# Optimization experiments

Measured on AMD Instinct MI355X. Metric: run time of the kernel, lower is better.

## Reference

```python
import jax, jax.numpy as jnp
import numpy as np

B, T, C, H, S = 4, 1024, 768, 12, 64  # batch, seq, emb_dim, n_heads, head_size
FF = 4 * C          # 3072, ff_hidden_size (required by SwiGLU input dim)
HID = int(8 * C / 3)  # 2048, SwiGLU hidden
EPS = 1e-6


def _rope_tables(seq_len, dim):
    # theta = 10000 ** (-2 * arange(0, dim, 2) / dim)  (note extra factor 2 vs standard RoPE)
    theta = 10000.0 ** (-2.0 * jnp.arange(0, dim, 2, dtype=jnp.float32) / dim)
    freqs = jnp.arange(seq_len, dtype=jnp.float32)[:, None] * theta  # [T, dim/2]
    cos = jnp.repeat(jnp.cos(freqs), 2, axis=-1)  # [T, dim]
    sin = jnp.repeat(jnp.sin(freqs), 2, axis=-1)
    return cos, sin


def _rope(x, cos, sin):
    # x: [..., T, S]; rotate pairs: even' = -odd, odd' = even
    rot = jnp.stack([-x[..., 1::2], x[..., 0::2]], axis=-1).reshape(x.shape)
    return x * cos + rot * sin


def _rmsnorm(x, gamma):
    # global scalar RMS over the whole tensor (faithful to torch.mean with no dim)
    return x / jnp.sqrt(EPS + jnp.mean(x * x)) * gamma


def _block(x, Wq, Wk, Wv, Wo, g1, g2, W1, b1, Ww, bw, Wg, bg, Wd, bd, W2, b2):
    Tlen = x.shape[1]
    cos, sin = _rope_tables(Tlen, S)
    # --- multi-head attention on rms1(x) ---
    h = _rmsnorm(x, g1)
    q = jnp.einsum('btc,hcs->bhts', h, Wq)
    k = jnp.einsum('btc,hcs->bhts', h, Wk)
    v = jnp.einsum('btc,hcs->bhts', h, Wv)
    rq = _rope(q, cos, sin)
    rk = _rope(k, cos, sin)
    scores = jnp.einsum('bhts,bhks->bhtk', rq, rk) * (C ** -0.5)  # scale by emb_dim, faithful
    causal = jnp.tril(jnp.ones((Tlen, Tlen), dtype=bool))
    scores = jnp.where(causal, scores, -jnp.inf)
    probs = jax.nn.softmax(scores, axis=-1)
    attn = jnp.einsum('bhtk,bhks->bhts', probs, v)
    attn = attn.transpose(0, 2, 1, 3).reshape(x.shape[0], Tlen, C)  # concat heads
    out = x + attn @ Wo
    # --- feed forward on rms2(out) ---
    h2 = _rmsnorm(out, g2)
    u = h2 @ W1 + b1                      # [B,T,FF]
    wx = u @ Ww + bw                      # [B,T,HID]
    vx = u @ Wg + bg
    ff = (wx * (vx * jax.nn.sigmoid(vx))) @ Wd + bd  # [B,T,FF]
    ff = ff @ W2 + b2                     # [B,T,C]
    return out + ff


def setup_inputs() -> dict:
    key = jax.random.key(0)
    ks = jax.random.split(key, 17)
    sd = 0.02
    return {
        'x':  jax.random.normal(ks[0], (B, T, C), jnp.float32),
        'Wq': jax.random.normal(ks[1], (H, C, S), jnp.float32) * sd,
        'Wk': jax.random.normal(ks[2], (H, C, S), jnp.float32) * sd,
        'Wv': jax.random.normal(ks[3], (H, C, S), jnp.float32) * sd,
        'Wo': jax.random.normal(ks[4], (C, C), jnp.float32) * sd,
        'g1': jnp.ones((C,), jnp.float32),
        'g2': jnp.ones((C,), jnp.float32),
        'W1': jax.random.normal(ks[5], (C, FF), jnp.float32) * sd,
        'b1': jnp.zeros((FF,), jnp.float32),
        'Ww': jax.random.normal(ks[6], (FF, HID), jnp.float32) * sd,
        'bw': jnp.zeros((HID,), jnp.float32),
        'Wg': jax.random.normal(ks[7], (FF, HID), jnp.float32) * sd,
        'bg': jnp.zeros((HID,), jnp.float32),
        'Wd': jax.random.normal(ks[8], (HID, FF), jnp.float32) * sd,
        'bd': jnp.zeros((FF,), jnp.float32),
        'W2': jax.random.normal(ks[9], (FF, C), jnp.float32) * sd,
        'b2': jnp.zeros((C,), jnp.float32),
    }


def reference(x, Wq, Wk, Wv, Wo, g1, g2, W1, b1, Ww, bw, Wg, bg, Wd, bd, W2, b2):
    return _block(x, Wq, Wk, Wv, Wo, g1, g2, W1, b1, Ww, bw, Wg, bg, Wd, bd, W2, b2)
```

## Files before the change

### kernel.cpp

```cpp
#include <hip/hip_runtime.h>
#include <math.h>

#define BB   4
#define TT   1024
#define CC   768
#define HH   12
#define SS   64
#define FFD  3072
#define HIDD 2048
#define NTOK (BB*TT)
#define EPSR 1e-6f

typedef __attribute__((ext_vector_type(8))) short bf16x8;
typedef __attribute__((ext_vector_type(4))) float f32x4;

__device__ __forceinline__ unsigned short f2bf(float f) {
    unsigned u = __float_as_uint(f);
    return (unsigned short)((u + 0x7FFFu + ((u >> 16) & 1u)) >> 16);
}
__device__ __forceinline__ float bfl(unsigned u) { return __uint_as_float(u << 16); }
__device__ __forceinline__ float bfh(unsigned u) { return __uint_as_float(u & 0xFFFF0000u); }
__device__ __forceinline__ unsigned pk2(float a, float b) {
    return (unsigned)f2bf(a) | ((unsigned)f2bf(b) << 16);
}

__device__ __forceinline__ void gload_lds16(const unsigned short* g, unsigned short* l) {
    __builtin_amdgcn_global_load_lds(
        (const __attribute__((address_space(1))) unsigned int*)g,
        (__attribute__((address_space(3))) unsigned int*)l, 16, 0, 0);
}

__global__ void k_sumsq_partial(const float* __restrict__ x, float* __restrict__ part, int n4) {
    __shared__ float sm[256];
    float s = 0.f;
    int stride = gridDim.x * blockDim.x;
    for (int i = blockIdx.x * blockDim.x + threadIdx.x; i < n4; i += stride) {
        float4 v = ((const float4*)x)[i];
        s += v.x*v.x + v.y*v.y + v.z*v.z + v.w*v.w;
    }
    sm[threadIdx.x] = s;
    __syncthreads();
    for (int off = 128; off > 0; off >>= 1) {
        if (threadIdx.x < off) sm[threadIdx.x] += sm[threadIdx.x + off];
        __syncthreads();
    }
    if (threadIdx.x == 0) part[blockIdx.x] = sm[0];
}

__global__ void k_scale_gamma_b(const float* __restrict__ x, const float* __restrict__ g,
                                const float* __restrict__ part, unsigned short* __restrict__ h,
                                int n8, float invn) {
    __shared__ float sm[256];
    float s = 0.f;
#pragma unroll
    for (int k = 0; k < 4; ++k) s += part[threadIdx.x + k*256];
    sm[threadIdx.x] = s;
    __syncthreads();
    for (int off = 128; off > 0; off >>= 1) {
        if (threadIdx.x < off) sm[threadIdx.x] += sm[threadIdx.x + off];
        __syncthreads();
    }
    float sc = 1.0f / sqrtf(EPSR + sm[0] * invn);
    int i = blockIdx.x * blockDim.x + threadIdx.x;
    if (i >= n8) return;
    float4 v0 = ((const float4*)x)[2*i];
    float4 v1 = ((const float4*)x)[2*i+1];
    int c = (i * 8) % CC;
    float4 g0 = *(const float4*)(g + c);
    float4 g1v = *(const float4*)(g + c + 4);
    uint4 r;
    r.x = pk2(v0.x*sc*g0.x,  v0.y*sc*g0.y);
    r.y = pk2(v0.z*sc*g0.z,  v0.w*sc*g0.w);
    r.z = pk2(v1.x*sc*g1v.x, v1.y*sc*g1v.y);
    r.w = pk2(v1.z*sc*g1v.z, v1.w*sc*g1v.w);
    ((uint4*)h)[i] = r;
}

#define TQKV 1728
#define TWO  576
#define TW1  2304
#define TWW  6144
#define TWD  6144
#define TW2  2304
#define J0 (TQKV)
#define J1 (J0 + TWO)
#define J2 (J1 + TW1)
#define J3 (J2 + TWW)
#define J4 (J3 + TWW)
#define J5 (J4 + TWD)
#define J6 (J5 + TW2)
#define J7 (J6 + 16)
#define J8 (J7 + 128)

__device__ __forceinline__ void wT_tile(float (*tl)[33], const float* __restrict__ W,
                                        unsigned short* __restrict__ Wt,
                                        int K, int N, int t, int tx, int ty) {
    int nk = K >> 5;
    int k0 = (t % nk) * 32, n0 = (t / nk) * 32;
#pragma unroll
    for (int i = 0; i < 4; ++i)
        tl[ty + i*8][tx] = W[(size_t)(k0 + ty + i*8) * N + n0 + tx];
    __syncthreads();
#pragma unroll
    for (int i = 0; i < 4; ++i)
        Wt[(size_t)(n0 + ty + i*8) * K + k0 + tx] = f2bf(tl[tx][ty + i*8]);
}

__global__ void k_prep(const float* __restrict__ Wq, const float* __restrict__ Wk,
                       const float* __restrict__ Wv, const float* __restrict__ Wo,
                       const float* __restrict__ W1, const float* __restrict__ Ww,
                       const float* __restrict__ Wg, const float* __restrict__ Wd,
                       const float* __restrict__ W2, const float* __restrict__ bw,
                       const float* __restrict__ bg,
                       unsigned short* __restrict__ wqkvT, unsigned short* __restrict__ WoT,
                       unsigned short* __restrict__ W1T, unsigned short* __restrict__ WcatT,
                       unsigned short* __restrict__ WdT, unsigned short* __restrict__ W2T,
                       float* __restrict__ bcat, float* __restrict__ tab) {
    __shared__ float tl[32][33];
    const int bid = blockIdx.x;
    const int tx = threadIdx.x & 31, ty = threadIdx.x >> 5;
    if (bid < J0) {
        int t = bid;
        int c0 = (t % 24) * 32;
        int s0 = ((t / 24) & 1) * 32;
        int z = t / 48, sel = z / HH, h = z % HH;
        const float* W = (sel == 0 ? Wq : (sel == 1 ? Wk : Wv)) + (size_t)h * CC * SS;
#pragma unroll
        for (int i = 0; i < 4; ++i)
            tl[ty + i*8][tx] = W[(size_t)(c0 + ty + i*8) * SS + s0 + tx];
        __syncthreads();
#pragma unroll
        for (int i = 0; i < 4; ++i)
            wqkvT[(size_t)(sel*CC + h*SS + s0 + ty + i*8) * CC + c0 + tx] = f2bf(tl[tx][ty + i*8]);
    } else if (bid < J1) {
        wT_tile(tl, Wo, WoT, CC, CC, bid - J0, tx, ty);
    } else if (bid < J2) {
        wT_tile(tl, W1, W1T, CC, FFD, bid - J1, tx, ty);
    } else if (bid < J3) {
        wT_tile(tl, Ww, WcatT, FFD, HIDD, bid - J2, tx, ty);
    } else if (bid < J4) {
        wT_tile(tl, Wg, WcatT + (size_t)HIDD*FFD, FFD, HIDD, bid - J3, tx, ty);
    } else if (bid < J5) {
        wT_tile(tl, Wd, WdT, HIDD, FFD, bid - J4, tx, ty);
    } else if (bid < J6) {
        wT_tile(tl, W2, W2T, FFD, CC, bid - J5, tx, ty);
    } else if (bid < J7) {
        int i = (bid - J6) * 256 + threadIdx.x;
        bcat[i] = (i < HIDD) ? bw[i] : bg[i - HIDD];
    } else {
        int i = (bid - J7) * 256 + threadIdx.x;
        int t = i >> 5, j = i & 31;
        float th = expf(-(float)j * 0.5756462732485115f);
        float ang = (float)t * th;
        tab[2*i]   = cosf(ang);
        tab[2*i+1] = sinf(ang);
    }
}

__global__ void k_rope_vt(unsigned short* __restrict__ qkv, const float* __restrict__ tab,
                          unsigned short* __restrict__ vtg) {
    const int bid = blockIdx.x;
    if (bid < 6144) {
        int i = bid * 256 + threadIdx.x;
        int j  = i & 31;
        int h  = (i >> 5) % HH;
        int bt = i / (32 * HH);
        int t  = bt & (TT - 1);
        float cs = tab[(t*32 + j)*2];
        float sn = tab[(t*32 + j)*2 + 1];
        size_t base = (size_t)bt * (3*CC) + h * SS + 2*j;
        unsigned q = *(unsigned*)(qkv + base);
        float qe = bfl(q), qo = bfh(q);
        *(unsigned*)(qkv + base) = pk2(qe*cs - qo*sn, qo*cs + qe*sn);
        unsigned k = *(unsigned*)(qkv + base + CC);
        float ke = bfl(k), ko = bfh(k);
        *(unsigned*)(qkv + base + CC) = pk2(ke*cs - ko*sn, ko*cs + ke*sn);
    } else {
        int b2 = bid - 6144;
        int bh = b2 >> 3, ty = b2 & 7;
        int b = bh / HH, h = bh % HH;
        int d = threadIdx.x & 63, tq = threadIdx.x >> 6;
        int t0 = ty * 128 + tq * 32;
        const unsigned short* src = qkv + (size_t)(b*TT + t0)*(3*CC) + 2*CC + h*SS + d;
        unsigned v[16];
#pragma unroll
        for (int e = 0; e < 16; ++e) {
            unsigned lo = src[(size_t)(2*e)*(3*CC)];
            unsigned hi = src[(size_t)(2*e+1)*(3*CC)];
            v[e] = (lo & 0xFFFFu) | (hi << 16);
        }
        uint4* dst = (uint4*)(vtg + ((size_t)bh*64 + d)*TT + t0);
#pragma unroll
        for (int q = 0; q < 4; ++q)
            dst[q] = make_uint4(v[q*4], v[q*4+1], v[q*4+2], v[q*4+3]);
    }
}

template<bool BIAS, bool RES, bool OUTB>
__global__ __launch_bounds__(256) void k_gemm_bf16(
    const unsigned short* __restrict__ A, const unsigned short* __restrict__ Bt,
    const float* __restrict__ bias, const float* __restrict__ res,
    void* __restrict__ Cv, int M, int N, int K)
{
    __shared__ unsigned short As[2][128*32];
    __shared__ unsigned short Bs[2][128*32];
    const int tid  = threadIdx.x;
    const int w    = tid >> 6, lane = tid & 63;
    const int wr   = w >> 1,  wc   = w & 1;
    const int row0 = blockIdx.y * 128, col0 = blockIdx.x * 128;

    f32x4 acc[4][4];
#pragma unroll
    for (int m = 0; m < 4; ++m)
#pragma unroll
        for (int n = 0; n < 4; ++n) acc[m][n] = (f32x4){0.f, 0.f, 0.f, 0.f};

    const int lr4 = lane >> 2;
    const int scb = lane & 3;

    auto stage = [&](int t, int buf) {
#pragma unroll
        for (int i = 0; i < 2; ++i) {
            int lr = w * 32 + i * 16 + lr4;
            int cbs = scb ^ ((lr >> 1) & 3);
            const unsigned short* ga = A + (size_t)(row0 + lr) * K + t * 32 + cbs * 8;
            gload_lds16(ga, &As[buf][(w * 32 + i * 16) * 32]);
            const unsigned short* gb = Bt + (size_t)(col0 + lr) * K + t * 32 + cbs * 8;
            gload_lds16(gb, &Bs[buf][(w * 32 + i * 16) * 32]);
        }
    };

    const int nt = K / 32;
    stage(0, 0);
    int cur = 0;
    const int fr = lane & 15, fq = lane >> 4;
    for (int t = 0; t < nt; ++t) {
        __syncthreads();
        if (t + 1 < nt) stage(t + 1, cur ^ 1);
        bf16x8 af[4], bf[4];
#pragma unroll
        for (int m = 0; m < 4; ++m) {
            int ra = wr * 64 + m * 16 + fr;
            af[m] = *(const bf16x8*)&As[cur][ra * 32 + (fq ^ ((ra >> 1) & 3)) * 8];
            int rb = wc * 64 + m * 16 + fr;
            bf[m] = *(const bf16x8*)&Bs[cur][rb * 32 + (fq ^ ((rb >> 1) & 3)) * 8];
        }
#pragma unroll
        for (int m = 0; m < 4; ++m)
#pragma unroll
            for (int n = 0; n < 4; ++n)
                acc[m][n] = __builtin_amdgcn_mfma_f32_16x16x32_bf16(af[m], bf[n], acc[m][n], 0, 0, 0);
        cur ^= 1;
    }

#pragma unroll
    for (int m = 0; m < 4; ++m) {
#pragma unroll
        for (int n = 0; n < 4; ++n) {
            int col = col0 + wc * 64 + n * 16 + fr;
            float bv = BIAS ? bias[col] : 0.f;
#pragma unroll
            for (int j = 0; j < 4; ++j) {
                int row = row0 + wr * 64 + m * 16 + fq * 4 + j;
                size_t off = (size_t)row * N + col;
                float v = acc[m][n][j] + bv;
                if (RES) v += res[off];
                if (OUTB) ((unsigned short*)Cv)[off] = f2bf(v);
                else      ((float*)Cv)[off] = v;
            }
        }
    }
}

#define GSTEP(s_, DOSTAGE, GATE)                                                  \
    {                                                                             \
        const int st_ = (s_) & 3;                                                 \
        const unsigned short* pa_ = &ringA[st_][0];                               \
        const unsigned short* pb_ = &ringB[st_][0];                               \
        bf16x8 af[8], bv[4];                                                      \
        _Pragma("unroll")                                                         \
        for (int m = 0; m < 8; ++m) {                                             \
            int ra = wm*128 + m*16 + fr;                                          \
            af[m] = *(const bf16x8*)&pa_[ra*32 + (fq ^ ((ra>>1)&3))*8];           \
        }                                                                         \
        _Pragma("unroll")                                                         \
        for (int n = 0; n < 4; ++n) {                                             \
            int rb = wn*64 + n*16 + fr;                                           \
            bv[n] = *(const bf16x8*)&pb_[rb*32 + (fq ^ ((rb>>1)&3))*8];           \
        }                                                                         \
        if (DOSTAGE) { stageA((s_) + 3); stageB((s_) + 3); }                      \
        asm volatile("s_waitcnt lgkmcnt(0)" ::: "memory");                        \
        __builtin_amdgcn_sched_barrier(0);                                        \
        __builtin_amdgcn_s_setprio(1);                                            \
        _Pragma("unroll")                                                         \
        for (int m = 0; m < 8; ++m)                                               \
            _Pragma("unroll")                                                     \
            for (int n = 0; n < 4; ++n)                                           \
                acc[m][n] = __builtin_amdgcn_mfma_f32_16x16x32_bf16(              \
                    af[m], bv[n], acc[m][n], 0, 0, 0);                            \
        __builtin_amdgcn_s_setprio(0);                                            \
        asm volatile("s_waitcnt " GATE ::: "memory");                             \
        __builtin_amdgcn_sched_barrier(0);                                        \
        __builtin_amdgcn_s_barrier();                                             \
    }

template<bool BIAS>
__global__ __launch_bounds__(512, 2) void k_gemm256(
    const unsigned short* __restrict__ A, const unsigned short* __restrict__ Bt,
    const float* __restrict__ bias, unsigned short* __restrict__ C,
    int M, int N, int K)
{
    __shared__ __align__(16) unsigned short ringA[4][256*32];
    __shared__ __align__(16) unsigned short ringB[4][256*32];
    const int tid = threadIdx.x;
    const int w = tid >> 6, lane = tid & 63;
    const int wm = w >> 2, wn = w & 3;
    const int fr = lane & 15, fq = lane >> 4;

    const int nwg = gridDim.x * gridDim.y;
    const int bid = blockIdx.y * gridDim.x + blockIdx.x;
    const int cpx = nwg >> 3;
    const int sbid = (bid & 7) * cpx + (bid >> 3);
    const int row0 = (sbid / gridDim.x) * 256;
    const int col0 = (sbid % gridDim.x) * 256;

    f32x4 acc[8][4];
#pragma unroll
    for (int m = 0; m < 8; ++m)
#pragma unroll
        for (int n = 0; n < 4; ++n) acc[m][n] = (f32x4){0.f, 0.f, 0.f, 0.f};

    auto stageA = [&](int t) {
        const int st = t & 3;
        const int kb = t * 32;
#pragma unroll
        for (int q = 0; q < 2; ++q) {
            int c = q * 512 + tid;
            int r = c >> 2;
            int part = (c & 3) ^ ((r >> 1) & 3);
            gload_lds16(A + (size_t)(row0 + r) * K + kb + part * 8,
                        &ringA[st][(q*512 + w*64) * 8]);
        }
    };
    auto stageB = [&](int t) {
        const int st = t & 3;
        const int kb = t * 32;
#pragma unroll
        for (int q = 0; q < 2; ++q) {
            int c = q * 512 + tid;
            int r = c >> 2;
            int part = (c & 3) ^ ((r >> 1) & 3);
            gload_lds16(Bt + (size_t)(col0 + r) * K + kb + part * 8,
                        &ringB[st][(q*512 + w*64) * 8]);
        }
    };

    const int S = K >> 5;
    stageA(0); stageB(0); stageA(1); stageB(1); stageA(2); stageB(2);
    asm volatile("s_waitcnt vmcnt(8)" ::: "memory");
    __builtin_amdgcn_s_barrier();
    int s = 0;
    for (; s < S - 3; ++s) GSTEP(s, true, "vmcnt(8)");
    GSTEP(s, false, "vmcnt(4)"); ++s;
    GSTEP(s, false, "vmcnt(0)"); ++s;
    GSTEP(s, false, "vmcnt(0)");

#pragma unroll
    for (int m = 0; m < 8; ++m) {
#pragma unroll
        for (int n = 0; n < 4; ++n) {
            int col = col0 + wn*64 + n*16 + fr;
            float bvb = BIAS ? bias[col] : 0.f;
#pragma unroll
            for (int j = 0; j < 4; ++j) {
                int row = row0 + wm*128 + m*16 + fq*4 + j;
                C[(size_t)row * N + col] = f2bf(acc[m][n][j] + bvb);
            }
        }
    }
}

__global__ __launch_bounds__(256) void k_attn_mfma(
    const unsigned short* __restrict__ qkv, const unsigned short* __restrict__ vtg,
    unsigned short* __restrict__ attn)
{
    __shared__ __align__(16) unsigned short Ks[2][64*64];
    __shared__ __align__(16) unsigned short Vs[2][64*64];
    __shared__ __align__(16) unsigned short Ps[4][16*72];
    const int tid = threadIdx.x;
    const int w = tid >> 6, lane = tid & 63;
    const int fr = lane & 15, fq = lane >> 4;
    const int bh = blockIdx.x, b = bh / HH, h = bh % HH;
    const int qb = blockIdx.y * 64;
    const int nkt = qb / 64 + 1;
    const float scale = 0.03608439182435161f;

    bf16x8 qf[2];
    {
        const unsigned short* qp = qkv + (size_t)(b*TT + qb + w*16 + fr)*(3*CC) + h*SS + fq*8;
        qf[0] = *(const bf16x8*)qp;
        qf[1] = *(const bf16x8*)(qp + 32);
    }

    auto stage = [&](int kt, int buf) {
        const unsigned short* kbase = qkv + (size_t)(b*TT + kt*64)*(3*CC) + CC + h*SS;
        const unsigned short* vbase = vtg + ((size_t)bh*64)*TT + kt*64;
#pragma unroll
        for (int p = 0; p < 2; ++p) {
            int s = p*256 + tid;
            int row = s >> 3;
            int blk = (s & 7) ^ (row & 7);
            gload_lds16(kbase + (size_t)row*(3*CC) + blk*8, &Ks[buf][(p*256 + w*64)*8]);
            gload_lds16(vbase + (size_t)row*TT + blk*8,     &Vs[buf][(p*256 + w*64)*8]);
        }
    };

    float m[4] = {-INFINITY, -INFINITY, -INFINITY, -INFINITY};
    float l[4] = {0.f, 0.f, 0.f, 0.f};
    f32x4 oacc[4];
#pragma unroll
    for (int n = 0; n < 4; ++n) oacc[n] = (f32x4){0.f, 0.f, 0.f, 0.f};

    stage(0, 0);
    int cur = 0;
    for (int kt = 0; kt < nkt; ++kt) {
        __syncthreads();
        if (kt + 1 < nkt) stage(kt + 1, cur ^ 1);

        f32x4 sacc[4];
#pragma unroll
        for (int n = 0; n < 4; ++n) sacc[n] = (f32x4){0.f, 0.f, 0.f, 0.f};
#pragma unroll
        for (int ks = 0; ks < 2; ++ks) {
#pragma unroll
            for (int n = 0; n < 4; ++n) {
                int row = n*16 + fr;
                bf16x8 kf = *(const bf16x8*)&Ks[cur][row*64 + ((ks*4 + fq) ^ (row & 7))*8];
                sacc[n] = __builtin_amdgcn_mfma_f32_16x16x32_bf16(qf[ks], kf, sacc[n], 0, 0, 0);
            }
        }

        float sv[4][4];
        const bool lastt = (kt == nkt - 1);
        const int qloc = w*16 + fq*4;
#pragma unroll
        for (int n = 0; n < 4; ++n) {
            int kloc = n*16 + fr;
#pragma unroll
            for (int j = 0; j < 4; ++j) {
                float vv = sacc[n][j] * scale;
                if (lastt && kloc > qloc + j) vv = -INFINITY;
                sv[j][n] = vv;
            }
        }
        float mx[4], ls[4];
#pragma unroll
        for (int j = 0; j < 4; ++j)
            mx[j] = fmaxf(fmaxf(sv[j][0], sv[j][1]), fmaxf(sv[j][2], sv[j][3]));
#pragma unroll
        for (int d = 1; d < 16; d <<= 1)
#pragma unroll
            for (int j = 0; j < 4; ++j) mx[j] = fmaxf(mx[j], __shfl_xor(mx[j], d));
        float corr[4];
#pragma unroll
        for (int j = 0; j < 4; ++j) {
            float nm = fmaxf(m[j], mx[j]);
            corr[j] = __expf(m[j] - nm);
            m[j] = nm;
        }
#pragma unroll
        for (int j = 0; j < 4; ++j) {
            float s0 = 0.f;
#pragma unroll
            for (int n = 0; n < 4; ++n) {
                float p = __expf(sv[j][n] - m[j]);
                sv[j][n] = p;
                s0 += p;
            }
            ls[j] = s0;
        }
#pragma unroll
        for (int d = 1; d < 16; d <<= 1)
#pragma unroll
            for (int j = 0; j < 4; ++j) ls[j] += __shfl_xor(ls[j], d);
#pragma unroll
        for (int j = 0; j < 4; ++j) l[j] = l[j]*corr[j] + ls[j];
#pragma unroll
        for (int n = 0; n < 4; ++n)
#pragma unroll
            for (int j = 0; j < 4; ++j) oacc[n][j] *= corr[j];

#pragma unroll
        for (int j = 0; j < 4; ++j)
#pragma unroll
            for (int n = 0; n < 4; ++n)
                Ps[w][(fq*4 + j)*72 + n*16 + fr] = f2bf(sv[j][n]);

#pragma unroll
        for (int ks = 0; ks < 2; ++ks) {
            bf16x8 pf = *(const bf16x8*)&Ps[w][fr*72 + ks*32 + fq*8];
#pragma unroll
            for (int n = 0; n < 4; ++n) {
                int row = n*16 + fr;
                bf16x8 vf = *(const bf16x8*)&Vs[cur][row*64 + ((ks*4 + fq) ^ (row & 7))*8];
                oacc[n] = __builtin_amdgcn_mfma_f32_16x16x32_bf16(pf, vf, oacc[n], 0, 0, 0);
            }
        }
        cur ^= 1;
    }

    float inv[4];
#pragma unroll
    for (int j = 0; j < 4; ++j) inv[j] = 1.0f / l[j];
#pragma unroll
    for (int n = 0; n < 4; ++n)
#pragma unroll
        for (int j = 0; j < 4; ++j) {
            size_t off = (size_t)(b*TT + qb + w*16 + fq*4 + j)*CC + h*SS + n*16 + fr;
            attn[off] = f2bf(oacc[n][j] * inv[j]);
        }
}

__global__ void k_swiglu_uv(const unsigned short* __restrict__ uv,
                            unsigned short* __restrict__ sw, int n8) {
    int i = blockIdx.x * blockDim.x + threadIdx.x;
    if (i >= n8) return;
    int r = i >> 8;
    int c8 = (i & 255) * 8;
    uint4 wv = *(const uint4*)(uv + (size_t)r * (2*HIDD) + c8);
    uint4 vv = *(const uint4*)(uv + (size_t)r * (2*HIDD) + HIDD + c8);
    uint4 rr;
    float w0, w1, v0, v1;
    w0 = bfl(wv.x); w1 = bfh(wv.x); v0 = bfl(vv.x); v1 = bfh(vv.x);
    rr.x = pk2(w0*v0/(1.f+__expf(-v0)), w1*v1/(1.f+__expf(-v1)));
    w0 = bfl(wv.y); w1 = bfh(wv.y); v0 = bfl(vv.y); v1 = bfh(vv.y);
    rr.y = pk2(w0*v0/(1.f+__expf(-v0)), w1*v1/(1.f+__expf(-v1)));
    w0 = bfl(wv.z); w1 = bfh(wv.z); v0 = bfl(vv.z); v1 = bfh(vv.z);
    rr.z = pk2(w0*v0/(1.f+__expf(-v0)), w1*v1/(1.f+__expf(-v1)));
    w0 = bfl(wv.w); w1 = bfh(wv.w); v0 = bfl(vv.w); v1 = bfh(vv.w);
    rr.w = pk2(w0*v0/(1.f+__expf(-v0)), w1*v1/(1.f+__expf(-v1)));
    *(uint4*)(sw + (size_t)r * HIDD + c8) = rr;
}

extern "C" void kernel_launch(void* const* d_in, const int* in_sizes, int n_in,
                              void* d_out, int out_size, void* d_ws, size_t ws_size,
                              hipStream_t stream)
{
    const float* x  = (const float*)d_in[0];
    const float* Wq = (const float*)d_in[1];
    const float* Wk = (const float*)d_in[2];
    const float* Wv = (const float*)d_in[3];
    const float* Wo = (const float*)d_in[4];
    const float* g1 = (const float*)d_in[5];
    const float* g2 = (const float*)d_in[6];
    const float* W1 = (const float*)d_in[7];
    const float* b1 = (const float*)d_in[8];
    const float* Ww = (const float*)d_in[9];
    const float* bw = (const float*)d_in[10];
    const float* Wg = (const float*)d_in[11];
    const float* bg = (const float*)d_in[12];
    const float* Wd = (const float*)d_in[13];
    const float* bd = (const float*)d_in[14];
    const float* W2 = (const float*)d_in[15];
    const float* b2 = (const float*)d_in[16];
    float* out = (float*)d_out;

    char* p = (char*)d_ws;
    auto alloc = [&](size_t bytes) { char* r = p; p += (bytes + 255) & ~(size_t)255; return r; };

    float*          part   = (float*)alloc(4096);
    float*          tab    = (float*)alloc((size_t)TT*32*2*4);
    float*          bcat   = (float*)alloc((size_t)2*HIDD*4);
    unsigned short* hb     = (unsigned short*)alloc((size_t)NTOK*CC*2);
    unsigned short* wqkvT  = (unsigned short*)alloc((size_t)3*CC*CC*2);
    unsigned short* qkvb   = (unsigned short*)alloc((size_t)NTOK*3*CC*2);
    unsigned short* vtg    = (unsigned short*)alloc((size_t)BB*HH*SS*TT*2);
    unsigned short* attnb  = (unsigned short*)alloc((size_t)NTOK*CC*2);
    unsigned short* WoT    = (unsigned short*)alloc((size_t)CC*CC*2);
    unsigned short* W1T    = (unsigned short*)alloc((size_t)FFD*CC*2);
    unsigned short* ub     = (unsigned short*)alloc((size_t)NTOK*FFD*2);
    unsigned short* WcatT  = (unsigned short*)alloc((size_t)2*HIDD*FFD*2);
    unsigned short* uvcat  = (unsigned short*)alloc((size_t)NTOK*2*HIDD*2);
    unsigned short* swb    = (unsigned short*)alloc((size_t)NTOK*HIDD*2);
    unsigned short* WdT    = (unsigned short*)alloc((size_t)FFD*HIDD*2);
    unsigned short* W2T    = (unsigned short*)alloc((size_t)CC*FFD*2);

    const int n = NTOK * CC;

    k_prep<<<J8, 256, 0, stream>>>(Wq, Wk, Wv, Wo, W1, Ww, Wg, Wd, W2, bw, bg,
                                   wqkvT, WoT, W1T, WcatT, WdT, W2T, bcat, tab);

    k_sumsq_partial<<<1024, 256, 0, stream>>>(x, part, n/4);
    k_scale_gamma_b<<<(n/8)/256, 256, 0, stream>>>(x, g1, part, hb, n/8, 1.0f/(float)n);

    k_gemm256<false><<<dim3(3*CC/256, NTOK/256), 512, 0, stream>>>(
        hb, wqkvT, nullptr, qkvb, NTOK, 3*CC, CC);
    k_rope_vt<<<6144 + 384, 256, 0, stream>>>(qkvb, tab, vtg);

    k_attn_mfma<<<dim3(BB*HH, TT/64), 256, 0, stream>>>(qkvb, vtg, attnb);

    k_gemm_bf16<false,true,false><<<dim3(CC/128, NTOK/128), 256, 0, stream>>>(
        attnb, WoT, nullptr, x, out, NTOK, CC, CC);

    k_sumsq_partial<<<1024, 256, 0, stream>>>(out, part, n/4);
    k_scale_gamma_b<<<(n/8)/256, 256, 0, stream>>>(out, g2, part, hb, n/8, 1.0f/(float)n);

    k_gemm256<true><<<dim3(FFD/256, NTOK/256), 512, 0, stream>>>(
        hb, W1T, b1, ub, NTOK, FFD, CC);
    k_gemm256<true><<<dim3(2*HIDD/256, NTOK/256), 512, 0, stream>>>(
        ub, WcatT, bcat, uvcat, NTOK, 2*HIDD, FFD);
    k_swiglu_uv<<<(NTOK*HIDD/8)/256, 256, 0, stream>>>(uvcat, swb, NTOK*HIDD/8);
    k_gemm256<true><<<dim3(FFD/256, NTOK/256), 512, 0, stream>>>(
        swb, WdT, bd, ub, NTOK, FFD, HIDD);
    k_gemm_bf16<true,true,false><<<dim3(CC/128, NTOK/128), 256, 0, stream>>>(
        ub, W2T, b2, out, out, NTOK, CC, FFD);
}
```

Measured before the change: 394.5 us.

## Fuse RMS sum-of-squares into prep and Wo GEMM; double-buffer LDS fragments in GEMM256

Removes the two standalone sum-of-squares kernels. The first RMS partial sums are folded into the weight-prep launch as extra blocks, and the second are computed in the epilogue of the Wo GEMM, followed by a per-block reduction. The 256-tile GEMM main loop now precomputes LDS offsets and source pointers and prefetches the next stage's fragments into a second register set, so LDS reads overlap the MFMAs under partial lgkm/vm waits. This costs more registers and an extra shared reduction in the Wo GEMM epilogue.

After: 391.8 us. About the same (-0.7%).

```diff
diff --git a/kernel.cpp b/kernel.cpp
--- a/kernel.cpp
+++ b/kernel.cpp
@@ -30,30 +30,12 @@
         (__attribute__((address_space(3))) unsigned int*)l, 16, 0, 0);
 }
 
-__global__ void k_sumsq_partial(const float* __restrict__ x, float* __restrict__ part, int n4) {
+__global__ void k_scale_gamma_b(const float* __restrict__ x, const float* __restrict__ g,
+                                const float* __restrict__ part, unsigned short* __restrict__ h,
+                                int n8, float invn, int npart) {
     __shared__ float sm[256];
     float s = 0.f;
-    int stride = gridDim.x * blockDim.x;
-    for (int i = blockIdx.x * blockDim.x + threadIdx.x; i < n4; i += stride) {
-        float4 v = ((const float4*)x)[i];
-        s += v.x*v.x + v.y*v.y + v.z*v.z + v.w*v.w;
-    }
-    sm[threadIdx.x] = s;
-    __syncthreads();
-    for (int off = 128; off > 0; off >>= 1) {
-        if (threadIdx.x < off) sm[threadIdx.x] += sm[threadIdx.x + off];
-        __syncthreads();
-    }
-    if (threadIdx.x == 0) part[blockIdx.x] = sm[0];
-}
-
-__global__ void k_scale_gamma_b(const float* __restrict__ x, const float* __restrict__ g,
-                                const float* __restrict__ part, unsigned short* __restrict__ h,
-                                int n8, float invn) {
-    __shared__ float sm[256];
-    float s = 0.f;
-#pragma unroll
-    for (int k = 0; k < 4; ++k) s += part[threadIdx.x + k*256];
+    for (int i = threadIdx.x; i < npart; i += 256) s += part[i];
     sm[threadIdx.x] = s;
     __syncthreads();
     for (int off = 128; off > 0; off >>= 1) {
@@ -91,6 +73,8 @@
 #define J6 (J5 + TW2)
 #define J7 (J6 + 16)
 #define J8 (J7 + 128)
+#define JSUM 1024
+#define J9 (J8 + JSUM)
 
 __device__ __forceinline__ void wT_tile(float (*tl)[33], const float* __restrict__ W,
                                         unsigned short* __restrict__ Wt,
@@ -111,11 +95,12 @@
                        const float* __restrict__ W1, const float* __restrict__ Ww,
                        const float* __restrict__ Wg, const float* __restrict__ Wd,
                        const float* __restrict__ W2, const float* __restrict__ bw,
-                       const float* __restrict__ bg,
+                       const float* __restrict__ bg, const float* __restrict__ x,
                        unsigned short* __restrict__ wqkvT, unsigned short* __restrict__ WoT,
                        unsigned short* __restrict__ W1T, unsigned short* __restrict__ WcatT,
                        unsigned short* __restrict__ WdT, unsigned short* __restrict__ W2T,
-                       float* __restrict__ bcat, float* __restrict__ tab) {
+                       float* __restrict__ bcat, float* __restrict__ tab,
+                       float* __restrict__ part) {
     __shared__ float tl[32][33];
     const int bid = blockIdx.x;
     const int tx = threadIdx.x & 31, ty = threadIdx.x >> 5;
@@ -147,13 +132,30 @@
     } else if (bid < J7) {
         int i = (bid - J6) * 256 + threadIdx.x;
         bcat[i] = (i < HIDD) ? bw[i] : bg[i - HIDD];
-    } else {
+    } else if (bid < J8) {
         int i = (bid - J7) * 256 + threadIdx.x;
         int t = i >> 5, j = i & 31;
         float th = expf(-(float)j * 0.5756462732485115f);
         float ang = (float)t * th;
         tab[2*i]   = cosf(ang);
         tab[2*i+1] = sinf(ang);
+    } else {
+        float* sm = &tl[0][0];
+        const int pb = bid - J8;
+        const int n4 = NTOK * CC / 4;
+        float s = 0.f;
+        int stride = JSUM * 256;
+        for (int i = pb * 256 + threadIdx.x; i < n4; i += stride) {
+            float4 v = ((const float4*)x)[i];
+            s += v.x*v.x + v.y*v.y + v.z*v.z + v.w*v.w;
+        }
+        sm[threadIdx.x] = s;
+        __syncthreads();
+        for (int off = 128; off > 0; off >>= 1) {
+            if (threadIdx.x < off) sm[threadIdx.x] += sm[threadIdx.x + off];
+            __syncthreads();
+        }
+        if (threadIdx.x == 0) part[pb] = sm[0];
     }
 }
 
@@ -196,14 +198,15 @@
     }
 }
 
-template<bool BIAS, bool RES, bool OUTB>
+template<bool BIAS, bool RES, bool OUTB, bool SSQ>
 __global__ __launch_bounds__(256) void k_gemm_bf16(
     const unsigned short* __restrict__ A, const unsigned short* __restrict__ Bt,
     const float* __restrict__ bias, const float* __restrict__ res,
-    void* __restrict__ Cv, int M, int N, int K)
+    void* __restrict__ Cv, int M, int N, int K, float* __restrict__ ssq_part)
 {
     __shared__ unsigned short As[2][128*32];
     __shared__ unsigned short Bs[2][128*32];
+    __shared__ float smr[256];
     const int tid  = threadIdx.x;
     const int w    = tid >> 6, lane = tid & 63;
     const int wr   = w >> 1,  wc   = w & 1;
@@ -253,6 +256,7 @@
         cur ^= 1;
     }
 
+    float ssq = 0.f;
 #pragma unroll
     for (int m = 0; m < 4; ++m) {
 #pragma unroll
@@ -267,29 +271,35 @@
                 if (RES) v += res[off];
                 if (OUTB) ((unsigned short*)Cv)[off] = f2bf(v);
                 else      ((float*)Cv)[off] = v;
+                if (SSQ) ssq += v * v;
             }
         }
     }
-}
-
-#define GSTEP(s_, DOSTAGE, GATE)                                                  \
+    if (SSQ) {
+        smr[tid] = ssq;
+        __syncthreads();
+        for (int off = 128; off > 0; off >>= 1) {
+            if (tid < off) smr[tid] += smr[tid + off];
+            __syncthreads();
+        }
+        if (tid == 0) ssq_part[blockIdx.y * gridDim.x + blockIdx.x] = smr[0];
+    }
+}
+
+#define INTERVAL(s_, RA, RB, NA, NB, DOSTAGE, DONEXT, LGKM, GATE)                 \
     {                                                                             \
-        const int st_ = (s_) & 3;                                                 \
-        const unsigned short* pa_ = &ringA[st_][0];                               \
-        const unsigned short* pb_ = &ringB[st_][0];                               \
-        bf16x8 af[8], bv[4];                                                      \
-        _Pragma("unroll")                                                         \
-        for (int m = 0; m < 8; ++m) {                                             \
-            int ra = wm*128 + m*16 + fr;                                          \
-            af[m] = *(const bf16x8*)&pa_[ra*32 + (fq ^ ((ra>>1)&3))*8];           \
-        }                                                                         \
-        _Pragma("unroll")                                                         \
-        for (int n = 0; n < 4; ++n) {                                             \
-            int rb = wn*64 + n*16 + fr;                                           \
-            bv[n] = *(const bf16x8*)&pb_[rb*32 + (fq ^ ((rb>>1)&3))*8];           \
+        if (DONEXT) {                                                             \
+            const int nx_ = ((s_) + 1) & 3;                                       \
+            _Pragma("unroll")                                                     \
+            for (int m = 0; m < 8; ++m)                                           \
+                NA[m] = *(const bf16x8*)&ringA[nx_][offA[m]];                     \
+            _Pragma("unroll")                                                     \
+            for (int n = 0; n < 4; ++n)                                           \
+                NB[n] = *(const bf16x8*)&ringB[nx_][offB[n]];                     \
         }                                                                         \
         if (DOSTAGE) { stageA((s_) + 3); stageB((s_) + 3); }                      \
-        asm volatile("s_waitcnt lgkmcnt(0)" ::: "memory");                        \
+        __builtin_amdgcn_sched_barrier(0);                                        \
+        asm volatile("s_waitcnt " LGKM ::: "memory");                             \
         __builtin_amdgcn_sched_barrier(0);                                        \
         __builtin_amdgcn_s_setprio(1);                                            \
         _Pragma("unroll")                                                         \
@@ -297,7 +307,7 @@
             _Pragma("unroll")                                                     \
             for (int n = 0; n < 4; ++n)                                           \
                 acc[m][n] = __builtin_amdgcn_mfma_f32_16x16x32_bf16(              \
-                    af[m], bv[n], acc[m][n], 0, 0, 0);                            \
+                    RA[m], RB[n], acc[m][n], 0, 0, 0);                            \
         __builtin_amdgcn_s_setprio(0);                                            \
         asm volatile("s_waitcnt " GATE ::: "memory");                             \
         __builtin_amdgcn_sched_barrier(0);                                        \
@@ -330,40 +340,59 @@
 #pragma unroll
         for (int n = 0; n < 4; ++n) acc[m][n] = (f32x4){0.f, 0.f, 0.f, 0.f};
 
+    const int c0 = tid, c1 = 512 + tid;
+    const int r0 = c0 >> 2, p0 = ((c0 & 3) ^ ((r0 >> 1) & 3)) * 8;
+    const int r1 = c1 >> 2, p1 = ((c1 & 3) ^ ((r1 >> 1) & 3)) * 8;
+    const unsigned short* aS0 = A  + (size_t)(row0 + r0) * K + p0;
+    const unsigned short* aS1 = A  + (size_t)(row0 + r1) * K + p1;
+    const unsigned short* bS0 = Bt + (size_t)(col0 + r0) * K + p0;
+    const unsigned short* bS1 = Bt + (size_t)(col0 + r1) * K + p1;
+    const int dL = w * 512;
     auto stageA = [&](int t) {
         const int st = t & 3;
         const int kb = t * 32;
-#pragma unroll
-        for (int q = 0; q < 2; ++q) {
-            int c = q * 512 + tid;
-            int r = c >> 2;
-            int part = (c & 3) ^ ((r >> 1) & 3);
-            gload_lds16(A + (size_t)(row0 + r) * K + kb + part * 8,
-                        &ringA[st][(q*512 + w*64) * 8]);
-        }
+        gload_lds16(aS0 + kb, &ringA[st][dL]);
+        gload_lds16(aS1 + kb, &ringA[st][4096 + dL]);
     };
     auto stageB = [&](int t) {
         const int st = t & 3;
         const int kb = t * 32;
-#pragma unroll
-        for (int q = 0; q < 2; ++q) {
-            int c = q * 512 + tid;
-            int r = c >> 2;
-            int part = (c & 3) ^ ((r >> 1) & 3);
-            gload_lds16(Bt + (size_t)(col0 + r) * K + kb + part * 8,
-                        &ringB[st][(q*512 + w*64) * 8]);
-        }
+        gload_lds16(bS0 + kb, &ringB[st][dL]);
+        gload_lds16(bS1 + kb, &ringB[st][4096 + dL]);
     };
+
+    int offA[8], offB[4];
+#pragma unroll
+    for (int m = 0; m < 8; ++m) {
+        int ra = wm*128 + m*16 + fr;
+        offA[m] = ra*32 + (fq ^ ((ra >> 1) & 3))*8;
+    }
+#pragma unroll
+    for (int n = 0; n < 4; ++n) {
+        int rb = wn*64 + n*16 + fr;
+        offB[n] = rb*32 + (fq ^ ((rb >> 1) & 3))*8;
+    }
 
     const int S = K >> 5;
     stageA(0); stageB(0); stageA(1); stageB(1); stageA(2); stageB(2);
-    asm volatile("s_waitcnt vmcnt(8)" ::: "memory");
+    asm volatile("s_waitcnt vmcnt(4)" ::: "memory");
     __builtin_amdgcn_s_barrier();
+
+    bf16x8 A0[8], B0[4], A1[8], B1[4];
+#pragma unroll
+    for (int m = 0; m < 8; ++m) A0[m] = *(const bf16x8*)&ringA[0][offA[m]];
+#pragma unroll
+    for (int n = 0; n < 4; ++n) B0[n] = *(const bf16x8*)&ringB[0][offB[n]];
+
     int s = 0;
-    for (; s < S - 3; ++s) GSTEP(s, true, "vmcnt(8)");
-    GSTEP(s, false, "vmcnt(4)"); ++s;
-    GSTEP(s, false, "vmcnt(0)"); ++s;
-    GSTEP(s, false, "vmcnt(0)");
+    for (; s < S - 4; s += 2) {
+        INTERVAL(s,   A0, B0, A1, B1, true, true, "lgkmcnt(12)", "vmcnt(4)");
+        INTERVAL(s+1, A1, B1, A0, B0, true, true, "lgkmcnt(12)", "vmcnt(4)");
+    }
+    INTERVAL(S-4, A0, B0, A1, B1, true,  true,  "lgkmcnt(12)", "vmcnt(4)");
+    INTERVAL(S-3, A1, B1, A0, B0, false, true,  "lgkmcnt(12)", "vmcnt(0)");
+    INTERVAL(S-2, A0, B0, A1, B1, false, true,  "lgkmcnt(12)", "vmcnt(0)");
+    INTERVAL(S-1, A1, B1, A0, B0, false, false, "lgkmcnt(0)",  "vmcnt(0)");
 
 #pragma unroll
     for (int m = 0; m < 8; ++m) {
@@ -587,11 +616,11 @@
 
     const int n = NTOK * CC;
 
-    k_prep<<<J8, 256, 0, stream>>>(Wq, Wk, Wv, Wo, W1, Ww, Wg, Wd, W2, bw, bg,
-                                   wqkvT, WoT, W1T, WcatT, WdT, W2T, bcat, tab);
-
-    k_sumsq_partial<<<1024, 256, 0, stream>>>(x, part, n/4);
-    k_scale_gamma_b<<<(n/8)/256, 256, 0, stream>>>(x, g1, part, hb, n/8, 1.0f/(float)n);
+    k_prep<<<J9, 256, 0, stream>>>(Wq, Wk, Wv, Wo, W1, Ww, Wg, Wd, W2, bw, bg, x,
+                                   wqkvT, WoT, W1T, WcatT, WdT, W2T, bcat, tab, part);
+
+    k_scale_gamma_b<<<(n/8)/256, 256, 0, stream>>>(x, g1, part, hb, n/8,
+                                                   1.0f/(float)n, JSUM);
 
     k_gemm256<false><<<dim3(3*CC/256, NTOK/256), 512, 0, stream>>>(
         hb, wqkvT, nullptr, qkvb, NTOK, 3*CC, CC);
@@ -599,11 +628,11 @@
 
     k_attn_mfma<<<dim3(BB*HH, TT/64), 256, 0, stream>>>(qkvb, vtg, attnb);
 
-    k_gemm_bf16<false,true,false><<<dim3(CC/128, NTOK/128), 256, 0, stream>>>(
-        attnb, WoT, nullptr, x, out, NTOK, CC, CC);
-
-    k_sumsq_partial<<<1024, 256, 0, stream>>>(out, part, n/4);
-    k_scale_gamma_b<<<(n/8)/256, 256, 0, stream>>>(out, g2, part, hb, n/8, 1.0f/(float)n);
+    k_gemm_bf16<false,true,false,true><<<dim3(CC/128, NTOK/128), 256, 0, stream>>>(
+        attnb, WoT, nullptr, x, out, NTOK, CC, CC, part);
+
+    k_scale_gamma_b<<<(n/8)/256, 256, 0, stream>>>(out, g2, part, hb, n/8,
+                                                   1.0f/(float)n, (CC/128)*(NTOK/128));
 
     k_gemm256<true><<<dim3(FFD/256, NTOK/256), 512, 0, stream>>>(
         hb, W1T, b1, ub, NTOK, FFD, CC);
@@ -612,6 +641,6 @@
     k_swiglu_uv<<<(NTOK*HIDD/8)/256, 256, 0, stream>>>(uvcat, swb, NTOK*HIDD/8);
     k_gemm256<true><<<dim3(FFD/256, NTOK/256), 512, 0, stream>>>(
         swb, WdT, bd, ub, NTOK, FFD, HIDD);
-    k_gemm_bf16<true,true,false><<<dim3(CC/128, NTOK/128), 256, 0, stream>>>(
-        ub, W2T, b2, out, out, NTOK, CC, FFD);
-}
+    k_gemm_bf16<true,true,false,false><<<dim3(CC/128, NTOK/128), 256, 0, stream>>>(
+        ub, W2T, b2, out, out, NTOK, CC, FFD, nullptr);
+}
```
